# Kernel tuning notes

Hardware: AMD Instinct MI355X
Metric: run time of the kernel (lower is better)

Reference implementation:

```python
import jax, jax.numpy as jnp
import numpy as np

B, T, N, H, E, LH, OUT, D = 64, 12, 325, 64, 32, 128, 12, 1
META_OFF = 65  # x[..., :1] is the signal, x[..., 65:] is the 32-dim temporal meta input


def _mlp(meta, W1, b1, W2, b2):
    # meta: (B,E); W1: (4,E,LH); W2: (4,LH,O) -> (4,B,O); 4 = gates g,i,f,o
    h = jax.nn.relu(jnp.einsum('be,geh->gbh', meta, W1) + b1[:, None, :])
    return jnp.einsum('gbh,gho->gbo', h, W2) + b2[:, None, :]


def setup_inputs() -> dict:
    key = jax.random.key(0)
    ks = jax.random.split(key, 16)
    s = lambda k, shape: jax.random.normal(k, shape, dtype=jnp.float32) * 0.05
    return {
        'x': jax.random.normal(ks[0], (B, T, N, 1 + 64 + E), dtype=jnp.float32),
        'lwx_W1': s(ks[1], (4, E, LH)), 'lwx_b1': s(ks[2], (4, LH)),
        'lwx_W2': s(ks[3], (4, LH, D * H)), 'lwx_b2': s(ks[4], (4, D * H)),
        'lwh_W1': s(ks[5], (4, E, LH)), 'lwh_b1': s(ks[6], (4, LH)),
        'lwh_W2': s(ks[7], (4, LH, H * H)), 'lwh_b2': s(ks[8], (4, H * H)),
        'lb_W1': s(ks[9], (4, E, LH)), 'lb_b1': s(ks[10], (4, LH)),
        'lb_W2': s(ks[11], (4, LH, H)), 'lb_b2': s(ks[12], (4, H)),
        'fc1_W': s(ks[13], (H, H // 2)), 'fc1_b': jnp.zeros((H // 2,), jnp.float32),
        'fc2_W': s(ks[14], (H // 2, OUT * D)), 'fc2_b': jnp.zeros((OUT * D,), jnp.float32),
    }


def reference(x, lwx_W1, lwx_b1, lwx_W2, lwx_b2,
              lwh_W1, lwh_b1, lwh_W2, lwh_b2,
              lb_W1, lb_b1, lb_W2, lb_b2,
              fc1_W, fc1_b, fc2_W, fc2_b):
    batch = x.shape[0]
    meta = jnp.mean(x[:, :, 0, META_OFF:], axis=1)  # (B,E)
    xs = jnp.transpose(x[..., :D], (1, 0, 2, 3))    # (T,B,N,D)

    Wx = _mlp(meta, lwx_W1, lwx_b1, lwx_W2, lwx_b2).reshape(4, batch, D, H)
    Wh = _mlp(meta, lwh_W1, lwh_b1, lwh_W2, lwh_b2).reshape(4, batch, H, H)
    b = _mlp(meta, lb_W1, lb_b1, lb_W2, lb_b2).reshape(4, batch, 1, H)

    def step(carry, xt):
        h, c = carry
        # (4,B,N,H): per-batch weights -> batched matmuls for all 4 gates
        z = (jnp.einsum('bnd,gbdh->gbnh', xt, Wx)
             + jnp.einsum('bnh,gbhk->gbnk', h, Wh) + b)
        g = jnp.tanh(z[0])
        i = jax.nn.sigmoid(z[1])
        f = jax.nn.sigmoid(z[2])
        o = jax.nn.sigmoid(z[3])
        c = g * i + c * f
        h = jnp.tanh(c) * o
        return (h, c), None

    # h0=c0=0 reproduces the torch t==0 special case exactly
    h0 = jnp.zeros((batch, N, H), x.dtype)
    (h, _), _ = jax.lax.scan(step, (h0, h0), xs)

    out = jax.nn.relu(h)
    out = jax.nn.relu(out @ fc1_W + fc1_b) @ fc2_W + fc2_b  # (B,N,OUT*D)
    out = out.reshape(batch, N, OUT, D)
    return jnp.transpose(out, (0, 2, 1, 3))  # (B,OUT,N,D)
```

## Files before the change

### kernel.cpp

```cpp
#include <hip/hip_runtime.h>
#include <stdint.h>

#define TT 12
#define NN 325
#define HH 64
#define EE 32
#define LHH 128
#define OO 12
#define CIN 97
#define MOFF 65
#define BB 64

typedef __attribute__((ext_vector_type(8))) short bf8;
typedef __attribute__((ext_vector_type(4))) float f4;

__device__ __forceinline__ float sigf(float x) {
  return __builtin_amdgcn_rcpf(1.f + __builtin_amdgcn_exp2f(-1.4426950408889634f * x));
}
__device__ __forceinline__ float tanhfast(float x) {
  return 1.f - 2.f * __builtin_amdgcn_rcpf(1.f + __builtin_amdgcn_exp2f(2.8853900817779268f * x));
}
__device__ __forceinline__ unsigned short f2bf(float f) {
  unsigned int u = __float_as_uint(f);
  u += 0x7fffu + ((u >> 16) & 1u);
  return (unsigned short)(u >> 16);
}

__global__ __launch_bounds__(256) void k_meta(
    const float* __restrict__ x,
    const float* __restrict__ xw1, const float* __restrict__ xb1,
    const float* __restrict__ xw2, const float* __restrict__ xb2,
    const float* __restrict__ hw1, const float* __restrict__ hb1,
    const float* __restrict__ bw1, const float* __restrict__ bb1,
    const float* __restrict__ bw2, const float* __restrict__ bb2,
    float* __restrict__ hid_ws, float* __restrict__ wx_ws,
    float* __restrict__ bg_ws)
{
  const int b = blockIdx.x, tid = threadIdx.x;
  __shared__ float meta_s[EE];
  __shared__ float hidx_s[512], hidb_s[512];

  if (tid < EE) {
    float s = 0.f;
    #pragma unroll
    for (int t = 0; t < TT; ++t)
      s += x[(size_t)((b * TT + t) * NN) * CIN + MOFF + tid];
    meta_s[tid] = s * (1.f / 12.f);
  }
  __syncthreads();

  for (int idx = tid; idx < 1536; idx += 256) {
    const int mlp = idx >> 9, rem = idx & 511;
    const int g = rem >> 7, l = rem & 127;
    const float* W1 = (mlp == 0) ? xw1 : ((mlp == 1) ? hw1 : bw1);
    const float* B1 = (mlp == 0) ? xb1 : ((mlp == 1) ? hb1 : bb1);
    float a = B1[rem];
    const float* w = W1 + g * (EE * LHH) + l;
    #pragma unroll
    for (int e = 0; e < EE; ++e) a = fmaf(meta_s[e], w[e * LHH], a);
    a = fmaxf(a, 0.f);
    if (mlp == 0) hidx_s[rem] = a;
    else if (mlp == 2) hidb_s[rem] = a;
    else hid_ws[g * (BB * LHH) + b * LHH + l] = a;
  }
  __syncthreads();

  {
    const int g = tid >> 6;
    const int h = tid & 63;
    float ax = xb2[tid];
    float ab = bb2[tid];
    const float* wxp = xw2 + (size_t)g * (LHH * HH) + h;
    const float* wbp = bw2 + (size_t)g * (LHH * HH) + h;
    const float* hx = hidx_s + g * LHH;
    const float* hb = hidb_s + g * LHH;
    #pragma unroll 8
    for (int l = 0; l < LHH; ++l) {
      ax = fmaf(hx[l], wxp[l * HH], ax);
      ab = fmaf(hb[l], wbp[l * HH], ab);
    }
    wx_ws[b * 256 + tid] = ax;
    bg_ws[b * 256 + tid] = ab;
  }
}

__global__ __launch_bounds__(256) void k_wh(
    const float* __restrict__ x,
    const float* __restrict__ hw2, const float* __restrict__ hb2,
    const float* __restrict__ hid_ws, unsigned short* __restrict__ whb,
    float* __restrict__ xg)
{
  const int g = blockIdx.x >> 6, i = blockIdx.x & 63, tid = threadIdx.x;
  __shared__ float hs[BB][132];
  __shared__ float w2s[LHH][HH];

  {
    const int base = blockIdx.x * 976;
    #pragma unroll
    for (int kk = 0; kk < 4; ++kk) {
      const int flat = base + kk * 256 + tid;
      if (flat < BB * TT * NN) {
        const int b = flat / (TT * NN);
        const int r = flat - b * (TT * NN);
        const int t = r / NN;
        const int n = r - t * NN;
        xg[flat] = x[(size_t)((b * TT + t) * NN + n) * CIN];
      }
    }
  }

  for (int idx = tid; idx < BB * LHH; idx += 256)
    hs[idx >> 7][idx & 127] = hid_ws[g * (BB * LHH) + idx];
  for (int idx = tid; idx < LHH * HH; idx += 256)
    w2s[idx >> 6][idx & 63] = hw2[(size_t)(g * LHH + (idx >> 6)) * 4096 + i * 64 + (idx & 63)];
  __syncthreads();

  const int rg = tid >> 4, cg = tid & 15;
  const int b0 = rg * 4, j0 = cg * 4;
  float acc[4][4] = {};
  for (int l = 0; l < LHH; l += 4) {
    f4 hv[4];
    #pragma unroll
    for (int rr = 0; rr < 4; ++rr) hv[rr] = *(const f4*)&hs[b0 + rr][l];
    #pragma unroll
    for (int ll = 0; ll < 4; ++ll) {
      const f4 wv = *(const f4*)&w2s[l + ll][j0];
      #pragma unroll
      for (int rr = 0; rr < 4; ++rr)
        #pragma unroll
        for (int jj = 0; jj < 4; ++jj)
          acc[rr][jj] = fmaf(hv[rr][ll], wv[jj], acc[rr][jj]);
    }
  }

  const int kh = i >> 5, quad = (i >> 3) & 3, j8 = i & 7;
  #pragma unroll
  for (int rr = 0; rr < 4; ++rr) {
    const int b = b0 + rr;
    #pragma unroll
    for (int jj = 0; jj < 4; ++jj) {
      const int j = j0 + jj;
      const float v = acc[rr][jj] + hb2[g * 4096 + i * 64 + j];
      const int col = g * 64 + j;
      const int nt = col >> 4, c16 = col & 15;
      const int lane = quad * 16 + c16;
      whb[(size_t)((b * 32 + kh * 16 + nt) * 64 + lane) * 8 + j8] = f2bf(v);
    }
  }
}

__global__ __launch_bounds__(256, 2) void k_lstm(
    const float* __restrict__ xg, const float* __restrict__ wx_ws,
    const float* __restrict__ bg_ws, const unsigned short* __restrict__ whb,
    const float* __restrict__ fc1W, const float* __restrict__ fc1b,
    const float* __restrict__ fc2W, const float* __restrict__ fc2b,
    float* __restrict__ out)
{
  const int rb = blockIdx.x, b = blockIdx.y, tid = threadIdx.x;
  const int wave = tid >> 6, lane = tid & 63, quad = lane >> 4, c16 = lane & 15;
  const int n0 = rb * 64;

  __shared__ __align__(16) unsigned short Hs[4][16][72];
  __shared__ float Xs[TT][64];
  __shared__ float fc1s[HH * 32];
  __shared__ float fc2s[32 * OO];
  __shared__ __align__(16) float HIDf[4][16][36];
  __shared__ float fc1bs[32];
  __shared__ float fc2bs[OO];

  for (int idx = tid; idx < TT * 64; idx += 256) {
    const int t = idx >> 6, r = idx & 63, n = n0 + r;
    Xs[t][r] = (n < NN) ? xg[b * (TT * NN) + t * NN + n] : 0.f;
  }
  for (int idx = tid; idx < HH * 32; idx += 256) fc1s[idx] = fc1W[idx];
  for (int idx = tid; idx < 32 * OO; idx += 256) fc2s[idx] = fc2W[idx];
  if (tid < 32) fc1bs[tid] = fc1b[tid];
  if (tid < OO) fc2bs[tid] = fc2b[tid];

  float wxv[16], bgv[16];
  #pragma unroll
  for (int nt = 0; nt < 16; ++nt) {
    wxv[nt] = wx_ws[b * 256 + nt * 16 + c16];
    bgv[nt] = bg_ws[b * 256 + nt * 16 + c16];
  }
  bf8 wf[2][16];
  #pragma unroll
  for (int kh = 0; kh < 2; ++kh)
    #pragma unroll
    for (int nt = 0; nt < 16; ++nt)
      wf[kh][nt] = *(const bf8*)(whb + (size_t)((b * 32 + kh * 16 + nt) * 64 + lane) * 8);

  float cst[16];
  #pragma unroll
  for (int q = 0; q < 16; ++q) cst[q] = 0.f;

  __syncthreads();

  #pragma unroll 1
  for (int t = 0; t < TT; ++t) {
    float xr[4];
    #pragma unroll
    for (int r = 0; r < 4; ++r) xr[r] = Xs[t][wave * 16 + quad * 4 + r];

    bf8 af0, af1;
    if (t > 0) {
      af0 = *(const bf8*)&Hs[wave][c16][quad * 8];
      af1 = *(const bf8*)&Hs[wave][c16][32 + quad * 8];
    }

    #pragma unroll
    for (int hc = 0; hc < 4; ++hc) {
      f4 a0, a1, a2, a3;
      #pragma unroll
      for (int r = 0; r < 4; ++r) {
        a0[r] = fmaf(xr[r], wxv[hc],      bgv[hc]);
        a1[r] = fmaf(xr[r], wxv[4 + hc],  bgv[4 + hc]);
        a2[r] = fmaf(xr[r], wxv[8 + hc],  bgv[8 + hc]);
        a3[r] = fmaf(xr[r], wxv[12 + hc], bgv[12 + hc]);
      }
      if (t > 0) {
        a0 = __builtin_amdgcn_mfma_f32_16x16x32_bf16(af0, wf[0][hc],      a0, 0, 0, 0);
        a0 = __builtin_amdgcn_mfma_f32_16x16x32_bf16(af1, wf[1][hc],      a0, 0, 0, 0);
        a1 = __builtin_amdgcn_mfma_f32_16x16x32_bf16(af0, wf[0][4 + hc],  a1, 0, 0, 0);
        a1 = __builtin_amdgcn_mfma_f32_16x16x32_bf16(af1, wf[1][4 + hc],  a1, 0, 0, 0);
        a2 = __builtin_amdgcn_mfma_f32_16x16x32_bf16(af0, wf[0][8 + hc],  a2, 0, 0, 0);
        a2 = __builtin_amdgcn_mfma_f32_16x16x32_bf16(af1, wf[1][8 + hc],  a2, 0, 0, 0);
        a3 = __builtin_amdgcn_mfma_f32_16x16x32_bf16(af0, wf[0][12 + hc], a3, 0, 0, 0);
        a3 = __builtin_amdgcn_mfma_f32_16x16x32_bf16(af1, wf[1][12 + hc], a3, 0, 0, 0);
      }
      #pragma unroll
      for (int r = 0; r < 4; ++r) {
        const float gg = tanhfast(a0[r]);
        const float ii = sigf(a1[r]);
        const float ff = sigf(a2[r]);
        const float oo = sigf(a3[r]);
        const float cc = fmaf(gg, ii, cst[hc * 4 + r] * ff);
        cst[hc * 4 + r] = cc;
        const float hh = tanhfast(cc) * oo;
        Hs[wave][quad * 4 + r][hc * 16 + c16] = f2bf(hh);
      }
    }
  }

  {
    const int row = c16;
    float hrow[HH];
    #pragma unroll
    for (int kc = 0; kc < 8; ++kc) {
      const bf8 hv = *(const bf8*)&Hs[wave][row][kc * 8];
      #pragma unroll
      for (int j = 0; j < 8; ++j) {
        const unsigned int us = (unsigned short)hv[j];
        hrow[kc * 8 + j] = fmaxf(__uint_as_float(us << 16), 0.f);
      }
    }
    float hid[8];
    #pragma unroll
    for (int uu = 0; uu < 8; ++uu) hid[uu] = fc1bs[quad * 8 + uu];
    #pragma unroll
    for (int k = 0; k < HH; ++k) {
      const float* wp = &fc1s[k * 32 + quad * 8];
      const f4 w0 = *(const f4*)wp;
      const f4 w1 = *(const f4*)(wp + 4);
      const float hk = hrow[k];
      hid[0] = fmaf(hk, w0[0], hid[0]);
      hid[1] = fmaf(hk, w0[1], hid[1]);
      hid[2] = fmaf(hk, w0[2], hid[2]);
      hid[3] = fmaf(hk, w0[3], hid[3]);
      hid[4] = fmaf(hk, w1[0], hid[4]);
      hid[5] = fmaf(hk, w1[1], hid[5]);
      hid[6] = fmaf(hk, w1[2], hid[6]);
      hid[7] = fmaf(hk, w1[3], hid[7]);
    }
    #pragma unroll
    for (int uu = 0; uu < 8; ++uu)
      HIDf[wave][row][quad * 8 + uu] = fmaxf(hid[uu], 0.f);
  }
  {
    const int row = c16;
    float o0 = fc2bs[quad * 3 + 0];
    float o1 = fc2bs[quad * 3 + 1];
    float o2 = fc2bs[quad * 3 + 2];
    #pragma unroll
    for (int k = 0; k < 32; ++k) {
      const float hvk = HIDf[wave][row][k];
      o0 = fmaf(hvk, fc2s[k * OO + quad * 3 + 0], o0);
      o1 = fmaf(hvk, fc2s[k * OO + quad * 3 + 1], o1);
      o2 = fmaf(hvk, fc2s[k * OO + quad * 3 + 2], o2);
    }
    const int n = n0 + wave * 16 + row;
    if (n < NN) {
      out[b * (OO * NN) + (quad * 3 + 0) * NN + n] = o0;
      out[b * (OO * NN) + (quad * 3 + 1) * NN + n] = o1;
      out[b * (OO * NN) + (quad * 3 + 2) * NN + n] = o2;
    }
  }
}

extern "C" void kernel_launch(void* const* d_in, const int* in_sizes, int n_in,
                              void* d_out, int out_size, void* d_ws, size_t ws_size,
                              hipStream_t stream) {
  const float* x    = (const float*)d_in[0];
  const float* xw1  = (const float*)d_in[1];
  const float* xb1  = (const float*)d_in[2];
  const float* xw2  = (const float*)d_in[3];
  const float* xb2  = (const float*)d_in[4];
  const float* hw1  = (const float*)d_in[5];
  const float* hb1  = (const float*)d_in[6];
  const float* hw2  = (const float*)d_in[7];
  const float* hb2  = (const float*)d_in[8];
  const float* bw1  = (const float*)d_in[9];
  const float* bb1  = (const float*)d_in[10];
  const float* bw2  = (const float*)d_in[11];
  const float* bb2  = (const float*)d_in[12];
  const float* fc1W = (const float*)d_in[13];
  const float* fc1b = (const float*)d_in[14];
  const float* fc2W = (const float*)d_in[15];
  const float* fc2b = (const float*)d_in[16];
  float* out = (float*)d_out;

  float* ws = (float*)d_ws;
  float* hid_ws = ws;
  float* wx_ws  = ws + 32768;
  float* bg_ws  = ws + 49152;
  float* xg_ws  = ws + 65536;
  unsigned short* whb = (unsigned short*)(ws + 65536 + BB * TT * NN);

  k_meta<<<64, 256, 0, stream>>>(x, xw1, xb1, xw2, xb2, hw1, hb1, bw1, bb1,
                                 bw2, bb2, hid_ws, wx_ws, bg_ws);
  k_wh<<<256, 256, 0, stream>>>(x, hw2, hb2, hid_ws, whb, xg_ws);
  k_lstm<<<dim3(6, 64), 256, 0, stream>>>(xg_ws, wx_ws, bg_ws, whb,
                                          fc1W, fc1b, fc2W, fc2b, out);
}
```

Measured before the change: 254.6 us.

## Split LSTM hidden columns across waves with 16-row blocks and per-step barriers

Restructures the LSTM kernel so each block handles 16 nodes instead of 64. Each of the four waves now computes 16 of the 64 hidden units for all four gates, exchanging h through a double-buffered LDS tile with a barrier every timestep. The grid grows from 384 to 1344 blocks, and per-thread registers drop (4 weight fragments instead of 32), which allows 4 blocks per CU. The aim is more parallelism and occupancy for a latency-bound recurrence, at the cost of per-step block synchronisation and redundant per-block loads of fc weights and Wh fragments. The FC head is also redistributed across all 256 threads.

```diff
diff --git a/kernel.cpp b/kernel.cpp
--- a/kernel.cpp
+++ b/kernel.cpp
@@ -24,6 +24,9 @@
   unsigned int u = __float_as_uint(f);
   u += 0x7fffu + ((u >> 16) & 1u);
   return (unsigned short)(u >> 16);
+}
+__device__ __forceinline__ float bf2f(unsigned short s) {
+  return __uint_as_float(((unsigned int)s) << 16);
 }
 
 __global__ __launch_bounds__(256) void k_meta(
@@ -149,7 +152,7 @@
   }
 }
 
-__global__ __launch_bounds__(256, 2) void k_lstm(
+__global__ __launch_bounds__(256, 4) void k_lstm(
     const float* __restrict__ xg, const float* __restrict__ wx_ws,
     const float* __restrict__ bg_ws, const unsigned short* __restrict__ whb,
     const float* __restrict__ fc1W, const float* __restrict__ fc1b,
@@ -158,18 +161,18 @@
 {
   const int rb = blockIdx.x, b = blockIdx.y, tid = threadIdx.x;
   const int wave = tid >> 6, lane = tid & 63, quad = lane >> 4, c16 = lane & 15;
-  const int n0 = rb * 64;
-
-  __shared__ __align__(16) unsigned short Hs[4][16][72];
-  __shared__ float Xs[TT][64];
+  const int n0 = rb * 16;
+
+  __shared__ __align__(16) unsigned short Hs[2][16][72];
+  __shared__ float Xs[TT][16];
   __shared__ float fc1s[HH * 32];
   __shared__ float fc2s[32 * OO];
-  __shared__ __align__(16) float HIDf[4][16][36];
+  __shared__ float HIDs[16][34];
   __shared__ float fc1bs[32];
   __shared__ float fc2bs[OO];
 
-  for (int idx = tid; idx < TT * 64; idx += 256) {
-    const int t = idx >> 6, r = idx & 63, n = n0 + r;
+  for (int idx = tid; idx < TT * 16; idx += 256) {
+    const int t = idx >> 4, r = idx & 15, n = n0 + r;
     Xs[t][r] = (n < NN) ? xg[b * (TT * NN) + t * NN + n] : 0.f;
   }
   for (int idx = tid; idx < HH * 32; idx += 256) fc1s[idx] = fc1W[idx];
@@ -177,22 +180,22 @@
   if (tid < 32) fc1bs[tid] = fc1b[tid];
   if (tid < OO) fc2bs[tid] = fc2b[tid];
 
-  float wxv[16], bgv[16];
+  float wxv[4], bgv[4];
   #pragma unroll
-  for (int nt = 0; nt < 16; ++nt) {
-    wxv[nt] = wx_ws[b * 256 + nt * 16 + c16];
-    bgv[nt] = bg_ws[b * 256 + nt * 16 + c16];
-  }
-  bf8 wf[2][16];
+  for (int g = 0; g < 4; ++g) {
+    wxv[g] = wx_ws[b * 256 + g * 64 + wave * 16 + c16];
+    bgv[g] = bg_ws[b * 256 + g * 64 + wave * 16 + c16];
+  }
+  bf8 wf[2][4];
   #pragma unroll
   for (int kh = 0; kh < 2; ++kh)
     #pragma unroll
-    for (int nt = 0; nt < 16; ++nt)
-      wf[kh][nt] = *(const bf8*)(whb + (size_t)((b * 32 + kh * 16 + nt) * 64 + lane) * 8);
-
-  float cst[16];
+    for (int g = 0; g < 4; ++g)
+      wf[kh][g] = *(const bf8*)(whb + (size_t)((b * 32 + kh * 16 + g * 4 + wave) * 64 + lane) * 8);
+
+  float cst[4];
   #pragma unroll
-  for (int q = 0; q < 16; ++q) cst[q] = 0.f;
+  for (int r = 0; r < 4; ++r) cst[r] = 0.f;
 
   __syncthreads();
 
@@ -200,100 +203,73 @@
   for (int t = 0; t < TT; ++t) {
     float xr[4];
     #pragma unroll
-    for (int r = 0; r < 4; ++r) xr[r] = Xs[t][wave * 16 + quad * 4 + r];
+    for (int r = 0; r < 4; ++r) xr[r] = Xs[t][quad * 4 + r];
 
     bf8 af0, af1;
     if (t > 0) {
-      af0 = *(const bf8*)&Hs[wave][c16][quad * 8];
-      af1 = *(const bf8*)&Hs[wave][c16][32 + quad * 8];
-    }
-
-    #pragma unroll
-    for (int hc = 0; hc < 4; ++hc) {
-      f4 a0, a1, a2, a3;
-      #pragma unroll
-      for (int r = 0; r < 4; ++r) {
-        a0[r] = fmaf(xr[r], wxv[hc],      bgv[hc]);
-        a1[r] = fmaf(xr[r], wxv[4 + hc],  bgv[4 + hc]);
-        a2[r] = fmaf(xr[r], wxv[8 + hc],  bgv[8 + hc]);
-        a3[r] = fmaf(xr[r], wxv[12 + hc], bgv[12 + hc]);
-      }
-      if (t > 0) {
-        a0 = __builtin_amdgcn_mfma_f32_16x16x32_bf16(af0, wf[0][hc],      a0, 0, 0, 0);
-        a0 = __builtin_amdgcn_mfma_f32_16x16x32_bf16(af1, wf[1][hc],      a0, 0, 0, 0);
-        a1 = __builtin_amdgcn_mfma_f32_16x16x32_bf16(af0, wf[0][4 + hc],  a1, 0, 0, 0);
-        a1 = __builtin_amdgcn_mfma_f32_16x16x32_bf16(af1, wf[1][4 + hc],  a1, 0, 0, 0);
-        a2 = __builtin_amdgcn_mfma_f32_16x16x32_bf16(af0, wf[0][8 + hc],  a2, 0, 0, 0);
-        a2 = __builtin_amdgcn_mfma_f32_16x16x32_bf16(af1, wf[1][8 + hc],  a2, 0, 0, 0);
-        a3 = __builtin_amdgcn_mfma_f32_16x16x32_bf16(af0, wf[0][12 + hc], a3, 0, 0, 0);
-        a3 = __builtin_amdgcn_mfma_f32_16x16x32_bf16(af1, wf[1][12 + hc], a3, 0, 0, 0);
-      }
-      #pragma unroll
-      for (int r = 0; r < 4; ++r) {
-        const float gg = tanhfast(a0[r]);
-        const float ii = sigf(a1[r]);
-        const float ff = sigf(a2[r]);
-        const float oo = sigf(a3[r]);
-        const float cc = fmaf(gg, ii, cst[hc * 4 + r] * ff);
-        cst[hc * 4 + r] = cc;
-        const float hh = tanhfast(cc) * oo;
-        Hs[wave][quad * 4 + r][hc * 16 + c16] = f2bf(hh);
-      }
-    }
+      af0 = *(const bf8*)&Hs[(t - 1) & 1][c16][quad * 8];
+      af1 = *(const bf8*)&Hs[(t - 1) & 1][c16][32 + quad * 8];
+    }
+
+    f4 a0, a1, a2, a3;
+    #pragma unroll
+    for (int r = 0; r < 4; ++r) {
+      a0[r] = fmaf(xr[r], wxv[0], bgv[0]);
+      a1[r] = fmaf(xr[r], wxv[1], bgv[1]);
+      a2[r] = fmaf(xr[r], wxv[2], bgv[2]);
+      a3[r] = fmaf(xr[r], wxv[3], bgv[3]);
+    }
+    if (t > 0) {
+      a0 = __builtin_amdgcn_mfma_f32_16x16x32_bf16(af0, wf[0][0], a0, 0, 0, 0);
+      a0 = __builtin_amdgcn_mfma_f32_16x16x32_bf16(af1, wf[1][0], a0, 0, 0, 0);
+      a1 = __builtin_amdgcn_mfma_f32_16x16x32_bf16(af0, wf[0][1], a1, 0, 0, 0);
+      a1 = __builtin_amdgcn_mfma_f32_16x16x32_bf16(af1, wf[1][1], a1, 0, 0, 0);
+      a2 = __builtin_amdgcn_mfma_f32_16x16x32_bf16(af0, wf[0][2], a2, 0, 0, 0);
+      a2 = __builtin_amdgcn_mfma_f32_16x16x32_bf16(af1, wf[1][2], a2, 0, 0, 0);
+      a3 = __builtin_amdgcn_mfma_f32_16x16x32_bf16(af0, wf[0][3], a3, 0, 0, 0);
+      a3 = __builtin_amdgcn_mfma_f32_16x16x32_bf16(af1, wf[1][3], a3, 0, 0, 0);
+    }
+    #pragma unroll
+    for (int r = 0; r < 4; ++r) {
+      const float gg = tanhfast(a0[r]);
+      const float ii = sigf(a1[r]);
+      const float ff = sigf(a2[r]);
+      const float oo = sigf(a3[r]);
+      const float cc = fmaf(gg, ii, cst[r] * ff);
+      cst[r] = cc;
+      const float hh = tanhfast(cc) * oo;
+      Hs[t & 1][quad * 4 + r][wave * 16 + c16] = f2bf(hh);
+    }
+    __syncthreads();
   }
 
   {
-    const int row = c16;
-    float hrow[HH];
+    const int row = tid & 15, uu = tid >> 4;
+    float h0 = fc1bs[2 * uu], h1 = fc1bs[2 * uu + 1];
     #pragma unroll
     for (int kc = 0; kc < 8; ++kc) {
-      const bf8 hv = *(const bf8*)&Hs[wave][row][kc * 8];
+      const bf8 hv = *(const bf8*)&Hs[1][row][kc * 8];
       #pragma unroll
       for (int j = 0; j < 8; ++j) {
-        const unsigned int us = (unsigned short)hv[j];
-        hrow[kc * 8 + j] = fmaxf(__uint_as_float(us << 16), 0.f);
+        const float hk = fmaxf(bf2f((unsigned short)hv[j]), 0.f);
+        const int k = kc * 8 + j;
+        h0 = fmaf(hk, fc1s[k * 32 + 2 * uu], h0);
+        h1 = fmaf(hk, fc1s[k * 32 + 2 * uu + 1], h1);
       }
     }
-    float hid[8];
-    #pragma unroll
-    for (int uu = 0; uu < 8; ++uu) hid[uu] = fc1bs[quad * 8 + uu];
-    #pragma unroll
-    for (int k = 0; k < HH; ++k) {
-      const float* wp = &fc1s[k * 32 + quad * 8];
-      const f4 w0 = *(const f4*)wp;
-      const f4 w1 = *(const f4*)(wp + 4);
-      const float hk = hrow[k];
-      hid[0] = fmaf(hk, w0[0], hid[0]);
-      hid[1] = fmaf(hk, w0[1], hid[1]);
-      hid[2] = fmaf(hk, w0[2], hid[2]);
-      hid[3] = fmaf(hk, w0[3], hid[3]);
-      hid[4] = fmaf(hk, w1[0], hid[4]);
-      hid[5] = fmaf(hk, w1[1], hid[5]);
-      hid[6] = fmaf(hk, w1[2], hid[6]);
-      hid[7] = fmaf(hk, w1[3], hid[7]);
-    }
-    #pragma unroll
-    for (int uu = 0; uu < 8; ++uu)
-      HIDf[wave][row][quad * 8 + uu] = fmaxf(hid[uu], 0.f);
-  }
-  {
-    const int row = c16;
-    float o0 = fc2bs[quad * 3 + 0];
-    float o1 = fc2bs[quad * 3 + 1];
-    float o2 = fc2bs[quad * 3 + 2];
-    #pragma unroll
-    for (int k = 0; k < 32; ++k) {
-      const float hvk = HIDf[wave][row][k];
-      o0 = fmaf(hvk, fc2s[k * OO + quad * 3 + 0], o0);
-      o1 = fmaf(hvk, fc2s[k * OO + quad * 3 + 1], o1);
-      o2 = fmaf(hvk, fc2s[k * OO + quad * 3 + 2], o2);
-    }
-    const int n = n0 + wave * 16 + row;
-    if (n < NN) {
-      out[b * (OO * NN) + (quad * 3 + 0) * NN + n] = o0;
-      out[b * (OO * NN) + (quad * 3 + 1) * NN + n] = o1;
-      out[b * (OO * NN) + (quad * 3 + 2) * NN + n] = o2;
-    }
+    HIDs[row][2 * uu] = fmaxf(h0, 0.f);
+    HIDs[row][2 * uu + 1] = fmaxf(h1, 0.f);
+  }
+  __syncthreads();
+  if (tid < 16 * OO) {
+    const int o = tid >> 4, row = tid & 15;
+    float acc = fc2bs[o];
+    #pragma unroll
+    for (int k = 0; k < 32; ++k)
+      acc = fmaf(HIDs[row][k], fc2s[k * OO + o], acc);
+    const int n = n0 + row;
+    if (n < NN)
+      out[b * (OO * NN) + o * NN + n] = acc;
   }
 }
 
@@ -329,6 +305,6 @@
   k_meta<<<64, 256, 0, stream>>>(x, xw1, xb1, xw2, xb2, hw1, hb1, bw1, bb1,
                                  bw2, bb2, hid_ws, wx_ws, bg_ws);
   k_wh<<<256, 256, 0, stream>>>(x, hw2, hb2, hid_ws, whb, xg_ws);
-  k_lstm<<<dim3(6, 64), 256, 0, stream>>>(xg_ws, wx_ws, bg_ws, whb,
-                                          fc1W, fc1b, fc2W, fc2b, out);
-}
+  k_lstm<<<dim3(21, 64), 256, 0, stream>>>(xg_ws, wx_ws, bg_ws, whb,
+                                           fc1W, fc1b, fc2W, fc2b, out);
+}
```

Result: faster. 224.9 us (-11.7%).
